# Performance work log

Measured on AMD Instinct MI355X. Metric: run time of the kernel, lower is better.

Reference implementation:

```python
import jax, jax.numpy as jnp
import numpy as np

N_NODES = 100000
N_EDGES = 1200000
N_GRAPHS = 1024
IN_FEATS = 64
HID = 64
BN_EPS = 1e-5


def setup_inputs() -> dict:
    key = jax.random.key(0)
    ks = jax.random.split(key, 20)
    feats = jax.random.normal(ks[0], (N_NODES, IN_FEATS), jnp.float32)
    src = jax.random.randint(ks[1], (N_EDGES,), 0, N_NODES, jnp.int32)
    dst = jax.random.randint(ks[2], (N_EDGES,), 0, N_NODES, jnp.int32)
    graph_ids = jnp.sort(jax.random.randint(ks[3], (N_NODES,), 0, N_GRAPHS, jnp.int32))

    def lin(k, fi, fo):
        s = 1.0 / np.sqrt(fi)
        kw, kb = jax.random.split(k)
        return (jax.random.uniform(kw, (fi, fo), jnp.float32, -s, s),
                jax.random.uniform(kb, (fo,), jnp.float32, -s, s))

    W_self, _ = lin(ks[4], IN_FEATS, HID)
    W_neigh, b_neigh = lin(ks[5], IN_FEATS, HID)
    W1, b1 = lin(ks[6], HID, 128)
    W2, b2 = lin(ks[7], 128, 64)
    W3, b3 = lin(ks[8], 64, 1)

    def bn(k, d):
        k1, k2, k3, k4 = jax.random.split(k, 4)
        return (jax.random.normal(k1, (d,), jnp.float32) * 0.1 + 1.0,
                jax.random.normal(k2, (d,), jnp.float32) * 0.1,
                jax.random.normal(k3, (d,), jnp.float32) * 0.1,
                jax.random.uniform(k4, (d,), jnp.float32, 0.5, 1.5))

    g1, be1, rm1, rv1 = bn(ks[9], 128)
    g2, be2, rm2, rv2 = bn(ks[10], 64)

    return dict(feats=feats, src=src, dst=dst, graph_ids=graph_ids,
                W_self=W_self, W_neigh=W_neigh, b_neigh=b_neigh,
                W1=W1, b1=b1, g1=g1, be1=be1, rm1=rm1, rv1=rv1,
                W2=W2, b2=b2, g2=g2, be2=be2, rm2=rm2, rv2=rv2,
                W3=W3, b3=b3)


def reference(feats, src, dst, graph_ids, W_self, W_neigh, b_neigh,
              W1, b1, g1, be1, rm1, rv1, W2, b2, g2, be2, rm2, rv2, W3, b3):
    # --- SAGEConv (mean aggregator): h = W_self@h_self + W_neigh@mean_neigh + b
    deg = jax.ops.segment_sum(jnp.ones((src.shape[0],), feats.dtype), dst,
                              num_segments=N_NODES)                      # [N]
    agg = jax.ops.segment_sum(feats[src], dst, num_segments=N_NODES)     # [N, F]
    mean_neigh = agg / jnp.maximum(deg, 1.0)[:, None]
    h = feats @ W_self + mean_neigh @ W_neigh + b_neigh
    h = jax.nn.relu(h)                                                   # activation

    # --- per-graph max readout (dgl.max_nodes)
    hg = jax.ops.segment_max(h, graph_ids, num_segments=N_GRAPHS)        # [G, HID]

    # --- MLP head with eval-mode BatchNorm1d
    def bn(x, g, b, rm, rv):
        return (x - rm) * jax.lax.rsqrt(rv + BN_EPS) * g + b

    x = bn(jax.nn.relu(hg @ W1 + b1), g1, be1, rm1, rv1)
    x = bn(jax.nn.relu(x @ W2 + b2), g2, be2, rm2, rv2)
    return x @ W3 + b3                                                   # [G, n_task]
```

## Files before the change

kernel.cpp:

```cpp
#include <hip/hip_runtime.h>
#include <hip/hip_fp16.h>

#define N_NODES  100000
#define N_EDGES  1200000
#define N_GRAPHS 1024
#define F        64
#define BN_EPS   1e-5f
#define NBUCK    ((N_NODES + 255) / 256)
#define NBLK     512
#define CHUNK    ((N_EDGES + NBLK - 1) / NBLK)
#define MT       128

__global__ __launch_bounds__(256) void chist(const int* __restrict__ dst,
                                             int* __restrict__ Ct,
                                             int* __restrict__ hgbits) {
  __shared__ int lh[NBUCK];
  int b = blockIdx.x, t = threadIdx.x;
  int zidx = b * 256 + t;
  if (zidx < N_GRAPHS * F) hgbits[zidx] = 0;
  for (int i = t; i < NBUCK; i += 256) lh[i] = 0;
  __syncthreads();
  int e0 = b * CHUNK, e1 = e0 + CHUNK;
  if (e1 > N_EDGES) e1 = N_EDGES;
  for (int e = e0 + t; e < e1; e += 256) atomicAdd(&lh[dst[e] >> 8], 1);
  __syncthreads();
  for (int i = t; i < NBUCK; i += 256) Ct[(size_t)b * NBUCK + i] = lh[i];
}

__global__ __launch_bounds__(NBLK) void cscan(int* __restrict__ Ct,
                                              int* __restrict__ bcnt) {
  __shared__ int s[NBLK];
  int i = blockIdx.x, t = threadIdx.x;
  int v = Ct[(size_t)t * NBUCK + i];
  s[t] = v;
  __syncthreads();
  for (int off = 1; off < NBLK; off <<= 1) {
    int u = (t >= off) ? s[t - off] : 0;
    __syncthreads();
    s[t] += u;
    __syncthreads();
  }
  Ct[(size_t)t * NBUCK + i] = s[t] - v;
  if (t == NBLK - 1) bcnt[i] = s[NBLK - 1];
}

__global__ __launch_bounds__(512) void bscan(const int* __restrict__ bcnt,
                                             int* __restrict__ bstart) {
  __shared__ int s[512];
  int t = threadIdx.x;
  int v = (t < NBUCK) ? bcnt[t] : 0;
  s[t] = v;
  __syncthreads();
  for (int off = 1; off < 512; off <<= 1) {
    int u = (t >= off) ? s[t - off] : 0;
    __syncthreads();
    s[t] += u;
    __syncthreads();
  }
  if (t < NBUCK) bstart[t] = s[t] - v;
  if (t == 0) bstart[NBUCK] = N_EDGES;
}

__global__ __launch_bounds__(256) void cscat(const int* __restrict__ src,
                                             const int* __restrict__ dst,
                                             const int* __restrict__ Ct,
                                             const int* __restrict__ bstart,
                                             int* __restrict__ pairs) {
  __shared__ int cur[NBUCK];
  int b = blockIdx.x, t = threadIdx.x;
  for (int i = t; i < NBUCK; i += 256)
    cur[i] = bstart[i] + Ct[(size_t)b * NBUCK + i];
  __syncthreads();
  int e0 = b * CHUNK, e1 = e0 + CHUNK;
  if (e1 > N_EDGES) e1 = N_EDGES;
  for (int e = e0 + t; e < e1; e += 256) {
    int d = dst[e];
    int pos = atomicAdd(&cur[d >> 8], 1);
    pairs[pos] = (int)((((unsigned)d & 255u) << 24) | (unsigned)src[e]);
  }
}

__global__ __launch_bounds__(256) void place(const int* __restrict__ pairs,
                                             const int* __restrict__ bstart,
                                             int* __restrict__ rs,
                                             int* __restrict__ eidx) {
  __shared__ int lh[256];
  __shared__ int cur[256];
  int b = blockIdx.x, t = threadIdx.x;
  int nb0 = b << 8;
  int r0 = bstart[b], r1 = bstart[b + 1];

  lh[t] = 0;
  __syncthreads();
  for (int e = r0 + t; e < r1; e += 256)
    atomicAdd(&lh[((unsigned)pairs[e]) >> 24], 1);
  __syncthreads();

  int v = lh[t];
  cur[t] = v;
  __syncthreads();
  for (int off = 1; off < 256; off <<= 1) {
    int u = (t >= off) ? cur[t - off] : 0;
    __syncthreads();
    cur[t] += u;
    __syncthreads();
  }
  int excl = cur[t] - v;
  int node = nb0 + t;
  if (node < N_NODES) rs[node] = r0 + excl;
  if (b == 0 && t == 0) rs[N_NODES] = N_EDGES;
  __syncthreads();
  cur[t] = r0 + excl;
  __syncthreads();

  for (int e = r0 + t; e < r1; e += 256) {
    unsigned p = (unsigned)pairs[e];
    int pos = atomicAdd(&cur[p >> 24], 1);
    eidx[pos] = (int)(p & 0xFFFFFFu);
  }
}

__global__ __launch_bounds__(256) void gemm_uz(
    const float* __restrict__ feats, const float* __restrict__ Wself,
    const float* __restrict__ Wneigh, __half* __restrict__ Uh,
    __half* __restrict__ Zh) {
  __shared__ float As[MT * 65];
  __shared__ float Ws[64 * 128];
  int t = threadIdx.x;
  int mbase = blockIdx.x * MT;

  for (int i = t; i < 64 * 128; i += 256) {
    int k = i >> 7, j = i & 127;
    Ws[i] = (j < 64) ? Wself[k * 64 + j] : Wneigh[k * 64 + (j - 64)];
  }
#pragma unroll
  for (int s = 0; s < 8; s++) {
    int idx = (s * 256 + t) * 4;
    int m = idx >> 6, k = idx & 63;
    int gm = mbase + m;
    float4 v = (gm < N_NODES) ? *(const float4*)(feats + (size_t)gm * F + k)
                              : make_float4(0.f, 0.f, 0.f, 0.f);
    float* d = As + m * 65 + k;
    d[0] = v.x; d[1] = v.y; d[2] = v.z; d[3] = v.w;
  }
  __syncthreads();

  int wave = t >> 6, lane = t & 63;
  int jq = lane & 3, nq = lane >> 2;
  int half = wave & 1;
  int mb = (wave >> 1) * 64 + 4 * nq;
  int joff = half * 64 + jq * 16;

  float acc[4][16];
#pragma unroll
  for (int i = 0; i < 4; i++)
#pragma unroll
    for (int c = 0; c < 16; c++) acc[i][c] = 0.f;

#pragma unroll 4
  for (int k = 0; k < 64; k++) {
    float a0 = As[(mb + 0) * 65 + k];
    float a1 = As[(mb + 1) * 65 + k];
    float a2 = As[(mb + 2) * 65 + k];
    float a3 = As[(mb + 3) * 65 + k];
    const float4* wr = (const float4*)(Ws + k * 128 + joff);
    float4 w4[4];
    w4[0] = wr[0]; w4[1] = wr[1]; w4[2] = wr[2]; w4[3] = wr[3];
    const float* w = (const float*)w4;
#pragma unroll
    for (int c = 0; c < 16; c++) {
      float wv = w[c];
      acc[0][c] += a0 * wv;
      acc[1][c] += a1 * wv;
      acc[2][c] += a2 * wv;
      acc[3][c] += a3 * wv;
    }
  }

  __half* outp = half ? Zh : Uh;
  int jbase = jq * 16;
#pragma unroll
  for (int i = 0; i < 4; i++) {
    int gm = mbase + mb + i;
    if (gm < N_NODES) {
#pragma unroll
      for (int c4 = 0; c4 < 4; c4++) {
        union { __half h[4]; uint2 u; } pk;
        pk.h[0] = __float2half_rn(acc[i][c4 * 4 + 0]);
        pk.h[1] = __float2half_rn(acc[i][c4 * 4 + 1]);
        pk.h[2] = __float2half_rn(acc[i][c4 * 4 + 2]);
        pk.h[3] = __float2half_rn(acc[i][c4 * 4 + 3]);
        *(uint2*)(outp + (size_t)gm * F + jbase + c4 * 4) = pk.u;
      }
    }
  }
}

__global__ __launch_bounds__(256) void gather_h(
    const __half* __restrict__ Uh, const __half* __restrict__ Zh,
    const int* __restrict__ rs, const int* __restrict__ eidx,
    const float* __restrict__ bneigh, const int* __restrict__ gids,
    int* __restrict__ hgbits) {
  int lane = threadIdx.x & 63;
  int wid  = (blockIdx.x * blockDim.x + threadIdx.x) >> 6;
  const int NW = (2048 * 256) >> 6;
  const int per = (N_NODES + NW - 1) / NW;
  int n0 = wid * per;
  int n1 = n0 + per; if (n1 > N_NODES) n1 = N_NODES;
  if (n0 >= n1) return;
  int fl  = lane & 15;
  int sub = lane >> 4;
  float4 b4 = *(const float4*)(bneigh + 4 * fl);

  int curg = gids[n0];
  float4 gmax = {0.f, 0.f, 0.f, 0.f};

  for (int n = n0; n < n1; n++) {
    uint2 ur = *(const uint2*)(Uh + (size_t)n * F + 4 * fl);
    int r0 = rs[n], r1 = rs[n + 1];
    float sx = 0.f, sy = 0.f, sz = 0.f, sw = 0.f;
    for (int base = r0; base < r1; base += 64) {
      int m = r1 - base; if (m > 64) m = 64;
      int myid = (lane < m) ? eidx[base + lane] : 0;
      for (int jj = 0; jj < m; jj += 16) {
        int j0 = jj + sub;
        int s0 = __shfl(myid, j0);
        int s1 = __shfl(myid, j0 + 4);
        int s2 = __shfl(myid, j0 + 8);
        int s3 = __shfl(myid, j0 + 12);
        uint2 z0 = *(const uint2*)(Zh + (size_t)s0 * F + 4 * fl);
        uint2 z1 = *(const uint2*)(Zh + (size_t)s1 * F + 4 * fl);
        uint2 z2 = *(const uint2*)(Zh + (size_t)s2 * F + 4 * fl);
        uint2 z3 = *(const uint2*)(Zh + (size_t)s3 * F + 4 * fl);
        if (j0 < m) {
          float2 f0 = __half22float2(*(__half2*)&z0.x);
          float2 f1 = __half22float2(*(__half2*)&z0.y);
          sx += f0.x; sy += f0.y; sz += f1.x; sw += f1.y;
        }
        if (j0 + 4 < m) {
          float2 f0 = __half22float2(*(__half2*)&z1.x);
          float2 f1 = __half22float2(*(__half2*)&z1.y);
          sx += f0.x; sy += f0.y; sz += f1.x; sw += f1.y;
        }
        if (j0 + 8 < m) {
          float2 f0 = __half22float2(*(__half2*)&z2.x);
          float2 f1 = __half22float2(*(__half2*)&z2.y);
          sx += f0.x; sy += f0.y; sz += f1.x; sw += f1.y;
        }
        if (j0 + 12 < m) {
          float2 f0 = __half22float2(*(__half2*)&z3.x);
          float2 f1 = __half22float2(*(__half2*)&z3.y);
          sx += f0.x; sy += f0.y; sz += f1.x; sw += f1.y;
        }
      }
    }
    sx += __shfl_xor(sx, 16); sy += __shfl_xor(sy, 16);
    sz += __shfl_xor(sz, 16); sw += __shfl_xor(sw, 16);
    sx += __shfl_xor(sx, 32); sy += __shfl_xor(sy, 32);
    sz += __shfl_xor(sz, 32); sw += __shfl_xor(sw, 32);
    float inv = 1.0f / fmaxf((float)(r1 - r0), 1.0f);

    int g = gids[n];
    if (g != curg) {
      if (sub == 0) {
        int* hp = hgbits + (size_t)curg * F + 4 * fl;
        atomicMax(hp + 0, __float_as_int(gmax.x));
        atomicMax(hp + 1, __float_as_int(gmax.y));
        atomicMax(hp + 2, __float_as_int(gmax.z));
        atomicMax(hp + 3, __float_as_int(gmax.w));
      }
      curg = g; gmax = make_float4(0.f, 0.f, 0.f, 0.f);
    }

    float2 uf0 = __half22float2(*(__half2*)&ur.x);
    float2 uf1 = __half22float2(*(__half2*)&ur.y);
    gmax.x = fmaxf(gmax.x, fmaxf(uf0.x + sx * inv + b4.x, 0.f));
    gmax.y = fmaxf(gmax.y, fmaxf(uf0.y + sy * inv + b4.y, 0.f));
    gmax.z = fmaxf(gmax.z, fmaxf(uf1.x + sz * inv + b4.z, 0.f));
    gmax.w = fmaxf(gmax.w, fmaxf(uf1.y + sw * inv + b4.w, 0.f));
  }
  if (sub == 0) {
    int* hp = hgbits + (size_t)curg * F + 4 * fl;
    atomicMax(hp + 0, __float_as_int(gmax.x));
    atomicMax(hp + 1, __float_as_int(gmax.y));
    atomicMax(hp + 2, __float_as_int(gmax.z));
    atomicMax(hp + 3, __float_as_int(gmax.w));
  }
}

#define GPB 8
__global__ __launch_bounds__(128) void mlp(
    const float* __restrict__ hg,
    const float* __restrict__ W1, const float* __restrict__ b1,
    const float* __restrict__ g1, const float* __restrict__ be1,
    const float* __restrict__ rm1, const float* __restrict__ rv1,
    const float* __restrict__ W2, const float* __restrict__ b2,
    const float* __restrict__ g2, const float* __restrict__ be2,
    const float* __restrict__ rm2, const float* __restrict__ rv2,
    const float* __restrict__ W3, const float* __restrict__ b3,
    float* __restrict__ out) {
  __shared__ float W1s[64 * 128];
  __shared__ float W2s[128 * 64];
  __shared__ float W3s[64];
  __shared__ float sc1[128], sh1[128], b1s[128];
  __shared__ float sc2[64],  sh2[64],  b2s[64];
  __shared__ float s0[64], s1[128], s2[64];
  int t = threadIdx.x;

  for (int i = t; i < 64 * 128; i += 128) W1s[i] = W1[i];
  for (int i = t; i < 128 * 64; i += 128) W2s[i] = W2[i];
  if (t < 64) W3s[t] = W3[t];
  {
    float iv = rsqrtf(rv1[t] + BN_EPS);
    float sc = g1[t] * iv;
    sc1[t] = sc; sh1[t] = be1[t] - rm1[t] * sc; b1s[t] = b1[t];
  }
  if (t < 64) {
    float iv = rsqrtf(rv2[t] + BN_EPS);
    float sc = g2[t] * iv;
    sc2[t] = sc; sh2[t] = be2[t] - rm2[t] * sc; b2s[t] = b2[t];
  }
  __syncthreads();

  for (int gg = 0; gg < GPB; gg++) {
    int g = blockIdx.x * GPB + gg;
    if (t < 64) s0[t] = hg[(size_t)g * F + t];
    __syncthreads();
    {
      float acc = b1s[t];
      for (int i = 0; i < 64; i++) acc += s0[i] * W1s[i * 128 + t];
      acc = fmaxf(acc, 0.0f);
      s1[t] = acc * sc1[t] + sh1[t];
    }
    __syncthreads();
    if (t < 64) {
      float acc = b2s[t];
      for (int i = 0; i < 128; i++) acc += s1[i] * W2s[i * 64 + t];
      acc = fmaxf(acc, 0.0f);
      s2[t] = acc * sc2[t] + sh2[t];
    }
    __syncthreads();
    if (t < 64) {
      float p = s2[t] * W3s[t];
      for (int off = 32; off > 0; off >>= 1) p += __shfl_down(p, off);
      if (t == 0) out[g] = p + b3[0];
    }
    __syncthreads();
  }
}

extern "C" void kernel_launch(void* const* d_in, const int* in_sizes, int n_in,
                              void* d_out, int out_size, void* d_ws, size_t ws_size,
                              hipStream_t stream) {
  const float* feats  = (const float*)d_in[0];
  const int*   src    = (const int*)d_in[1];
  const int*   dst    = (const int*)d_in[2];
  const int*   gids   = (const int*)d_in[3];
  const float* Wself  = (const float*)d_in[4];
  const float* Wneigh = (const float*)d_in[5];
  const float* bneigh = (const float*)d_in[6];
  const float* W1  = (const float*)d_in[7];
  const float* b1  = (const float*)d_in[8];
  const float* g1  = (const float*)d_in[9];
  const float* be1 = (const float*)d_in[10];
  const float* rm1 = (const float*)d_in[11];
  const float* rv1 = (const float*)d_in[12];
  const float* W2  = (const float*)d_in[13];
  const float* b2  = (const float*)d_in[14];
  const float* g2  = (const float*)d_in[15];
  const float* be2 = (const float*)d_in[16];
  const float* rm2 = (const float*)d_in[17];
  const float* rv2 = (const float*)d_in[18];
  const float* W3  = (const float*)d_in[19];
  const float* b3  = (const float*)d_in[20];

  __half* Uh   = (__half*)d_ws;
  __half* Zh   = Uh + (size_t)N_NODES * F;
  int* rs      = (int*)(Zh + (size_t)N_NODES * F);
  int* bstart  = rs + (N_NODES + 1);
  int* bcnt    = bstart + (NBUCK + 1);
  int* hgbits  = bcnt + NBUCK;
  int* Ct      = hgbits + (size_t)N_GRAPHS * F;
  int* pairs   = Ct + (size_t)NBLK * NBUCK;
  int* eidx    = pairs + N_EDGES;

  chist<<<NBLK, 256, 0, stream>>>(dst, Ct, hgbits);
  cscan<<<NBUCK, NBLK, 0, stream>>>(Ct, bcnt);
  bscan<<<1, 512, 0, stream>>>(bcnt, bstart);
  cscat<<<NBLK, 256, 0, stream>>>(src, dst, Ct, bstart, pairs);
  gemm_uz<<<(N_NODES + MT - 1) / MT, 256, 0, stream>>>(feats, Wself, Wneigh,
                                                       Uh, Zh);
  place<<<NBUCK, 256, 0, stream>>>(pairs, bstart, rs, eidx);
  gather_h<<<2048, 256, 0, stream>>>(Uh, Zh, rs, eidx, bneigh, gids, hgbits);
  mlp<<<N_GRAPHS / GPB, 128, 0, stream>>>((const float*)hgbits,
                                          W1, b1, g1, be1, rm1, rv1,
                                          W2, b2, g2, be2, rm2, rv2, W3, b3,
                                          (float*)d_out);
}
```

Baseline: 230.1 us.

## Fuse CSR placement into bucket-level gather with shared-memory atomic accumulation

```diff
diff --git a/kernel.cpp b/kernel.cpp
--- a/kernel.cpp
+++ b/kernel.cpp
@@ -10,6 +10,8 @@
 #define NBLK     512
 #define CHUNK    ((N_EDGES + NBLK - 1) / NBLK)
 #define MT       128
+#define GS       32
+#define ASTRIDE  68
 
 __global__ __launch_bounds__(256) void chist(const int* __restrict__ dst,
                                              int* __restrict__ Ct,
@@ -77,46 +79,6 @@
     int d = dst[e];
     int pos = atomicAdd(&cur[d >> 8], 1);
     pairs[pos] = (int)((((unsigned)d & 255u) << 24) | (unsigned)src[e]);
-  }
-}
-
-__global__ __launch_bounds__(256) void place(const int* __restrict__ pairs,
-                                             const int* __restrict__ bstart,
-                                             int* __restrict__ rs,
-                                             int* __restrict__ eidx) {
-  __shared__ int lh[256];
-  __shared__ int cur[256];
-  int b = blockIdx.x, t = threadIdx.x;
-  int nb0 = b << 8;
-  int r0 = bstart[b], r1 = bstart[b + 1];
-
-  lh[t] = 0;
-  __syncthreads();
-  for (int e = r0 + t; e < r1; e += 256)
-    atomicAdd(&lh[((unsigned)pairs[e]) >> 24], 1);
-  __syncthreads();
-
-  int v = lh[t];
-  cur[t] = v;
-  __syncthreads();
-  for (int off = 1; off < 256; off <<= 1) {
-    int u = (t >= off) ? cur[t - off] : 0;
-    __syncthreads();
-    cur[t] += u;
-    __syncthreads();
-  }
-  int excl = cur[t] - v;
-  int node = nb0 + t;
-  if (node < N_NODES) rs[node] = r0 + excl;
-  if (b == 0 && t == 0) rs[N_NODES] = N_EDGES;
-  __syncthreads();
-  cur[t] = r0 + excl;
-  __syncthreads();
-
-  for (int e = r0 + t; e < r1; e += 256) {
-    unsigned p = (unsigned)pairs[e];
-    int pos = atomicAdd(&cur[p >> 24], 1);
-    eidx[pos] = (int)(p & 0xFFFFFFu);
   }
 }
 
@@ -196,95 +158,83 @@
   }
 }
 
-__global__ __launch_bounds__(256) void gather_h(
+__global__ __launch_bounds__(256) void gather_agg(
     const __half* __restrict__ Uh, const __half* __restrict__ Zh,
-    const int* __restrict__ rs, const int* __restrict__ eidx,
+    const int* __restrict__ pairs, const int* __restrict__ bstart,
     const float* __restrict__ bneigh, const int* __restrict__ gids,
     int* __restrict__ hgbits) {
-  int lane = threadIdx.x & 63;
-  int wid  = (blockIdx.x * blockDim.x + threadIdx.x) >> 6;
-  const int NW = (2048 * 256) >> 6;
-  const int per = (N_NODES + NW - 1) / NW;
-  int n0 = wid * per;
-  int n1 = n0 + per; if (n1 > N_NODES) n1 = N_NODES;
-  if (n0 >= n1) return;
-  int fl  = lane & 15;
-  int sub = lane >> 4;
-  float4 b4 = *(const float4*)(bneigh + 4 * fl);
-
-  int curg = gids[n0];
-  float4 gmax = {0.f, 0.f, 0.f, 0.f};
-
-  for (int n = n0; n < n1; n++) {
-    uint2 ur = *(const uint2*)(Uh + (size_t)n * F + 4 * fl);
-    int r0 = rs[n], r1 = rs[n + 1];
-    float sx = 0.f, sy = 0.f, sz = 0.f, sw = 0.f;
-    for (int base = r0; base < r1; base += 64) {
-      int m = r1 - base; if (m > 64) m = 64;
-      int myid = (lane < m) ? eidx[base + lane] : 0;
-      for (int jj = 0; jj < m; jj += 16) {
-        int j0 = jj + sub;
-        int s0 = __shfl(myid, j0);
-        int s1 = __shfl(myid, j0 + 4);
-        int s2 = __shfl(myid, j0 + 8);
-        int s3 = __shfl(myid, j0 + 12);
-        uint2 z0 = *(const uint2*)(Zh + (size_t)s0 * F + 4 * fl);
-        uint2 z1 = *(const uint2*)(Zh + (size_t)s1 * F + 4 * fl);
-        uint2 z2 = *(const uint2*)(Zh + (size_t)s2 * F + 4 * fl);
-        uint2 z3 = *(const uint2*)(Zh + (size_t)s3 * F + 4 * fl);
-        if (j0 < m) {
-          float2 f0 = __half22float2(*(__half2*)&z0.x);
-          float2 f1 = __half22float2(*(__half2*)&z0.y);
-          sx += f0.x; sy += f0.y; sz += f1.x; sw += f1.y;
-        }
-        if (j0 + 4 < m) {
-          float2 f0 = __half22float2(*(__half2*)&z1.x);
-          float2 f1 = __half22float2(*(__half2*)&z1.y);
-          sx += f0.x; sy += f0.y; sz += f1.x; sw += f1.y;
-        }
-        if (j0 + 8 < m) {
-          float2 f0 = __half22float2(*(__half2*)&z2.x);
-          float2 f1 = __half22float2(*(__half2*)&z2.y);
-          sx += f0.x; sy += f0.y; sz += f1.x; sw += f1.y;
-        }
-        if (j0 + 12 < m) {
-          float2 f0 = __half22float2(*(__half2*)&z3.x);
-          float2 f1 = __half22float2(*(__half2*)&z3.y);
-          sx += f0.x; sy += f0.y; sz += f1.x; sw += f1.y;
-        }
+  __shared__ float acc[256 * ASTRIDE];
+  __shared__ int   degh[256];
+  __shared__ int   gmaxl[GS * 64];
+  int b = blockIdx.x, t = threadIdx.x;
+  int nb0 = b << 8;
+  int nbkt = N_NODES - nb0; if (nbkt > 256) nbkt = 256;
+  int r0 = bstart[b], r1 = bstart[b + 1];
+
+  for (int i = t; i < 256 * ASTRIDE; i += 256) acc[i] = 0.f;
+  degh[t] = 0;
+  for (int i = t; i < GS * 64; i += 256) gmaxl[i] = 0;
+  __syncthreads();
+
+  int q  = t & 15;
+  int eg = t >> 4;
+
+  for (int e = r0 + eg; e < r1; e += 16) {
+    unsigned p = (unsigned)pairs[e];
+    int ld  = (int)(p >> 24);
+    int sid = (int)(p & 0xFFFFFFu);
+    uint2 z = *(const uint2*)(Zh + (size_t)sid * F + 4 * q);
+    float2 f0 = __half22float2(*(__half2*)&z.x);
+    float2 f1 = __half22float2(*(__half2*)&z.y);
+    float* a = acc + ld * ASTRIDE + 4 * q;
+    atomicAdd(a + 0, f0.x);
+    atomicAdd(a + 1, f0.y);
+    atomicAdd(a + 2, f1.x);
+    atomicAdd(a + 3, f1.y);
+    if (q == 0) atomicAdd(&degh[ld], 1);
+  }
+  __syncthreads();
+
+  float4 b4 = *(const float4*)(bneigh + 4 * q);
+  int gid0 = gids[nb0];
+#pragma unroll
+  for (int pass = 0; pass < 16; pass++) {
+    int nl = eg + pass * 16;
+    if (nl < nbkt) {
+      int node = nb0 + nl;
+      float inv = 1.0f / fmaxf((float)degh[nl], 1.0f);
+      uint2 u = *(const uint2*)(Uh + (size_t)node * F + 4 * q);
+      float2 u0 = __half22float2(*(__half2*)&u.x);
+      float2 u1 = __half22float2(*(__half2*)&u.y);
+      const float* a = acc + nl * ASTRIDE + 4 * q;
+      float hx = fmaxf(u0.x + a[0] * inv + b4.x, 0.f);
+      float hy = fmaxf(u0.y + a[1] * inv + b4.y, 0.f);
+      float hz = fmaxf(u1.x + a[2] * inv + b4.z, 0.f);
+      float hw = fmaxf(u1.y + a[3] * inv + b4.w, 0.f);
+      int slot = gids[node] - gid0;
+      if (slot < GS) {
+        int* gm = gmaxl + slot * 64 + 4 * q;
+        atomicMax(gm + 0, __float_as_int(hx));
+        atomicMax(gm + 1, __float_as_int(hy));
+        atomicMax(gm + 2, __float_as_int(hz));
+        atomicMax(gm + 3, __float_as_int(hw));
+      } else {
+        int* hp = hgbits + (size_t)gids[node] * F + 4 * q;
+        atomicMax(hp + 0, __float_as_int(hx));
+        atomicMax(hp + 1, __float_as_int(hy));
+        atomicMax(hp + 2, __float_as_int(hz));
+        atomicMax(hp + 3, __float_as_int(hw));
       }
     }
-    sx += __shfl_xor(sx, 16); sy += __shfl_xor(sy, 16);
-    sz += __shfl_xor(sz, 16); sw += __shfl_xor(sw, 16);
-    sx += __shfl_xor(sx, 32); sy += __shfl_xor(sy, 32);
-    sz += __shfl_xor(sz, 32); sw += __shfl_xor(sw, 32);
-    float inv = 1.0f / fmaxf((float)(r1 - r0), 1.0f);
-
-    int g = gids[n];
-    if (g != curg) {
-      if (sub == 0) {
-        int* hp = hgbits + (size_t)curg * F + 4 * fl;
-        atomicMax(hp + 0, __float_as_int(gmax.x));
-        atomicMax(hp + 1, __float_as_int(gmax.y));
-        atomicMax(hp + 2, __float_as_int(gmax.z));
-        atomicMax(hp + 3, __float_as_int(gmax.w));
-      }
-      curg = g; gmax = make_float4(0.f, 0.f, 0.f, 0.f);
-    }
-
-    float2 uf0 = __half22float2(*(__half2*)&ur.x);
-    float2 uf1 = __half22float2(*(__half2*)&ur.y);
-    gmax.x = fmaxf(gmax.x, fmaxf(uf0.x + sx * inv + b4.x, 0.f));
-    gmax.y = fmaxf(gmax.y, fmaxf(uf0.y + sy * inv + b4.y, 0.f));
-    gmax.z = fmaxf(gmax.z, fmaxf(uf1.x + sz * inv + b4.z, 0.f));
-    gmax.w = fmaxf(gmax.w, fmaxf(uf1.y + sw * inv + b4.w, 0.f));
-  }
-  if (sub == 0) {
-    int* hp = hgbits + (size_t)curg * F + 4 * fl;
-    atomicMax(hp + 0, __float_as_int(gmax.x));
-    atomicMax(hp + 1, __float_as_int(gmax.y));
-    atomicMax(hp + 2, __float_as_int(gmax.z));
-    atomicMax(hp + 3, __float_as_int(gmax.w));
+  }
+  __syncthreads();
+
+  for (int i = t; i < GS * 64; i += 256) {
+    int v = gmaxl[i];
+    if (v != 0) {
+      int slot = i >> 6, f = i & 63;
+      atomicMax(&hgbits[(size_t)(gid0 + slot) * F + f], v);
+    }
   }
 }
 
@@ -376,13 +326,11 @@
 
   __half* Uh   = (__half*)d_ws;
   __half* Zh   = Uh + (size_t)N_NODES * F;
-  int* rs      = (int*)(Zh + (size_t)N_NODES * F);
-  int* bstart  = rs + (N_NODES + 1);
+  int* bstart  = (int*)(Zh + (size_t)N_NODES * F);
   int* bcnt    = bstart + (NBUCK + 1);
   int* hgbits  = bcnt + NBUCK;
   int* Ct      = hgbits + (size_t)N_GRAPHS * F;
   int* pairs   = Ct + (size_t)NBLK * NBUCK;
-  int* eidx    = pairs + N_EDGES;
 
   chist<<<NBLK, 256, 0, stream>>>(dst, Ct, hgbits);
   cscan<<<NBUCK, NBLK, 0, stream>>>(Ct, bcnt);
@@ -390,8 +338,8 @@
   cscat<<<NBLK, 256, 0, stream>>>(src, dst, Ct, bstart, pairs);
   gemm_uz<<<(N_NODES + MT - 1) / MT, 256, 0, stream>>>(feats, Wself, Wneigh,
                                                        Uh, Zh);
-  place<<<NBUCK, 256, 0, stream>>>(pairs, bstart, rs, eidx);
-  gather_h<<<2048, 256, 0, stream>>>(Uh, Zh, rs, eidx, bneigh, gids, hgbits);
+  gather_agg<<<NBUCK, 256, 0, stream>>>(Uh, Zh, pairs, bstart, bneigh,
+                                        gids, hgbits);
   mlp<<<N_GRAPHS / GPB, 128, 0, stream>>>((const float*)hgbits,
                                           W1, b1, g1, be1, rm1, rv1,
                                           W2, b2, g2, be2, rm2, rv2, W3, b3,
```

Result: slower. 703.2 us (+205.6%).

## Fuse histogram into GEMM launch and process four nodes per wavefront in gather

Applied to the files above, without the earlier changes.

```diff
diff --git a/kernel.cpp b/kernel.cpp
--- a/kernel.cpp
+++ b/kernel.cpp
@@ -10,123 +10,33 @@
 #define NBLK     512
 #define CHUNK    ((N_EDGES + NBLK - 1) / NBLK)
 #define MT       128
-
-__global__ __launch_bounds__(256) void chist(const int* __restrict__ dst,
-                                             int* __restrict__ Ct,
-                                             int* __restrict__ hgbits) {
-  __shared__ int lh[NBUCK];
-  int b = blockIdx.x, t = threadIdx.x;
-  int zidx = b * 256 + t;
-  if (zidx < N_GRAPHS * F) hgbits[zidx] = 0;
-  for (int i = t; i < NBUCK; i += 256) lh[i] = 0;
-  __syncthreads();
-  int e0 = b * CHUNK, e1 = e0 + CHUNK;
-  if (e1 > N_EDGES) e1 = N_EDGES;
-  for (int e = e0 + t; e < e1; e += 256) atomicAdd(&lh[dst[e] >> 8], 1);
-  __syncthreads();
-  for (int i = t; i < NBUCK; i += 256) Ct[(size_t)b * NBUCK + i] = lh[i];
-}
-
-__global__ __launch_bounds__(NBLK) void cscan(int* __restrict__ Ct,
-                                              int* __restrict__ bcnt) {
-  __shared__ int s[NBLK];
-  int i = blockIdx.x, t = threadIdx.x;
-  int v = Ct[(size_t)t * NBUCK + i];
-  s[t] = v;
-  __syncthreads();
-  for (int off = 1; off < NBLK; off <<= 1) {
-    int u = (t >= off) ? s[t - off] : 0;
-    __syncthreads();
-    s[t] += u;
-    __syncthreads();
-  }
-  Ct[(size_t)t * NBUCK + i] = s[t] - v;
-  if (t == NBLK - 1) bcnt[i] = s[NBLK - 1];
-}
-
-__global__ __launch_bounds__(512) void bscan(const int* __restrict__ bcnt,
-                                             int* __restrict__ bstart) {
-  __shared__ int s[512];
-  int t = threadIdx.x;
-  int v = (t < NBUCK) ? bcnt[t] : 0;
-  s[t] = v;
-  __syncthreads();
-  for (int off = 1; off < 512; off <<= 1) {
-    int u = (t >= off) ? s[t - off] : 0;
-    __syncthreads();
-    s[t] += u;
-    __syncthreads();
-  }
-  if (t < NBUCK) bstart[t] = s[t] - v;
-  if (t == 0) bstart[NBUCK] = N_EDGES;
-}
-
-__global__ __launch_bounds__(256) void cscat(const int* __restrict__ src,
-                                             const int* __restrict__ dst,
-                                             const int* __restrict__ Ct,
-                                             const int* __restrict__ bstart,
-                                             int* __restrict__ pairs) {
-  __shared__ int cur[NBUCK];
-  int b = blockIdx.x, t = threadIdx.x;
-  for (int i = t; i < NBUCK; i += 256)
-    cur[i] = bstart[i] + Ct[(size_t)b * NBUCK + i];
-  __syncthreads();
-  int e0 = b * CHUNK, e1 = e0 + CHUNK;
-  if (e1 > N_EDGES) e1 = N_EDGES;
-  for (int e = e0 + t; e < e1; e += 256) {
-    int d = dst[e];
-    int pos = atomicAdd(&cur[d >> 8], 1);
-    pairs[pos] = (int)((((unsigned)d & 255u) << 24) | (unsigned)src[e]);
-  }
-}
-
-__global__ __launch_bounds__(256) void place(const int* __restrict__ pairs,
-                                             const int* __restrict__ bstart,
-                                             int* __restrict__ rs,
-                                             int* __restrict__ eidx) {
-  __shared__ int lh[256];
-  __shared__ int cur[256];
-  int b = blockIdx.x, t = threadIdx.x;
-  int nb0 = b << 8;
-  int r0 = bstart[b], r1 = bstart[b + 1];
-
-  lh[t] = 0;
-  __syncthreads();
-  for (int e = r0 + t; e < r1; e += 256)
-    atomicAdd(&lh[((unsigned)pairs[e]) >> 24], 1);
-  __syncthreads();
-
-  int v = lh[t];
-  cur[t] = v;
-  __syncthreads();
-  for (int off = 1; off < 256; off <<= 1) {
-    int u = (t >= off) ? cur[t - off] : 0;
-    __syncthreads();
-    cur[t] += u;
-    __syncthreads();
-  }
-  int excl = cur[t] - v;
-  int node = nb0 + t;
-  if (node < N_NODES) rs[node] = r0 + excl;
-  if (b == 0 && t == 0) rs[N_NODES] = N_EDGES;
-  __syncthreads();
-  cur[t] = r0 + excl;
-  __syncthreads();
-
-  for (int e = r0 + t; e < r1; e += 256) {
-    unsigned p = (unsigned)pairs[e];
-    int pos = atomicAdd(&cur[p >> 24], 1);
-    eidx[pos] = (int)(p & 0xFFFFFFu);
-  }
-}
-
-__global__ __launch_bounds__(256) void gemm_uz(
+#define GEMM_BLOCKS ((N_NODES + MT - 1) / MT)
+
+__global__ __launch_bounds__(256) void prep(
     const float* __restrict__ feats, const float* __restrict__ Wself,
     const float* __restrict__ Wneigh, __half* __restrict__ Uh,
-    __half* __restrict__ Zh) {
-  __shared__ float As[MT * 65];
-  __shared__ float Ws[64 * 128];
+    __half* __restrict__ Zh, const int* __restrict__ dst,
+    int* __restrict__ Ct, int* __restrict__ hgbits) {
+  __shared__ __align__(16) char smraw[MT * 65 * 4 + 64 * 128 * 4];
   int t = threadIdx.x;
+
+  if (blockIdx.x >= GEMM_BLOCKS) {
+    int* lh = (int*)smraw;
+    int b = blockIdx.x - GEMM_BLOCKS;
+    int zidx = b * 256 + t;
+    if (zidx < N_GRAPHS * F) hgbits[zidx] = 0;
+    for (int i = t; i < NBUCK; i += 256) lh[i] = 0;
+    __syncthreads();
+    int e0 = b * CHUNK, e1 = e0 + CHUNK;
+    if (e1 > N_EDGES) e1 = N_EDGES;
+    for (int e = e0 + t; e < e1; e += 256) atomicAdd(&lh[dst[e] >> 8], 1);
+    __syncthreads();
+    for (int i = t; i < NBUCK; i += 256) Ct[(size_t)b * NBUCK + i] = lh[i];
+    return;
+  }
+
+  float* As = (float*)smraw;
+  float* Ws = (float*)(smraw + MT * 65 * 4);
   int mbase = blockIdx.x * MT;
 
   for (int i = t; i < 64 * 128; i += 256) {
@@ -193,6 +103,99 @@
         *(uint2*)(outp + (size_t)gm * F + jbase + c4 * 4) = pk.u;
       }
     }
+  }
+}
+
+__global__ __launch_bounds__(NBLK) void cscan(int* __restrict__ Ct,
+                                              int* __restrict__ bcnt) {
+  __shared__ int s[NBLK];
+  int i = blockIdx.x, t = threadIdx.x;
+  int v = Ct[(size_t)t * NBUCK + i];
+  s[t] = v;
+  __syncthreads();
+  for (int off = 1; off < NBLK; off <<= 1) {
+    int u = (t >= off) ? s[t - off] : 0;
+    __syncthreads();
+    s[t] += u;
+    __syncthreads();
+  }
+  Ct[(size_t)t * NBUCK + i] = s[t] - v;
+  if (t == NBLK - 1) bcnt[i] = s[NBLK - 1];
+}
+
+__global__ __launch_bounds__(512) void bscan(const int* __restrict__ bcnt,
+                                             int* __restrict__ bstart) {
+  __shared__ int s[512];
+  int t = threadIdx.x;
+  int v = (t < NBUCK) ? bcnt[t] : 0;
+  s[t] = v;
+  __syncthreads();
+  for (int off = 1; off < 512; off <<= 1) {
+    int u = (t >= off) ? s[t - off] : 0;
+    __syncthreads();
+    s[t] += u;
+    __syncthreads();
+  }
+  if (t < NBUCK) bstart[t] = s[t] - v;
+  if (t == 0) bstart[NBUCK] = N_EDGES;
+}
+
+__global__ __launch_bounds__(256) void cscat(const int* __restrict__ src,
+                                             const int* __restrict__ dst,
+                                             const int* __restrict__ Ct,
+                                             const int* __restrict__ bstart,
+                                             int* __restrict__ pairs) {
+  __shared__ int cur[NBUCK];
+  int b = blockIdx.x, t = threadIdx.x;
+  for (int i = t; i < NBUCK; i += 256)
+    cur[i] = bstart[i] + Ct[(size_t)b * NBUCK + i];
+  __syncthreads();
+  int e0 = b * CHUNK, e1 = e0 + CHUNK;
+  if (e1 > N_EDGES) e1 = N_EDGES;
+  for (int e = e0 + t; e < e1; e += 256) {
+    int d = dst[e];
+    int pos = atomicAdd(&cur[d >> 8], 1);
+    pairs[pos] = (int)((((unsigned)d & 255u) << 24) | (unsigned)src[e]);
+  }
+}
+
+__global__ __launch_bounds__(256) void place(const int* __restrict__ pairs,
+                                             const int* __restrict__ bstart,
+                                             int* __restrict__ rs,
+                                             int* __restrict__ eidx) {
+  __shared__ int lh[256];
+  __shared__ int cur[256];
+  int b = blockIdx.x, t = threadIdx.x;
+  int nb0 = b << 8;
+  int r0 = bstart[b], r1 = bstart[b + 1];
+
+  lh[t] = 0;
+  __syncthreads();
+  for (int e = r0 + t; e < r1; e += 256)
+    atomicAdd(&lh[((unsigned)pairs[e]) >> 24], 1);
+  __syncthreads();
+
+  int v = lh[t];
+  cur[t] = v;
+  __syncthreads();
+  for (int off = 1; off < 256; off <<= 1) {
+    int u = (t >= off) ? cur[t - off] : 0;
+    __syncthreads();
+    cur[t] += u;
+    __syncthreads();
+  }
+  int excl = cur[t] - v;
+  int node = nb0 + t;
+  if (node < N_NODES) rs[node] = r0 + excl;
+  if (b == 0 && t == 0) rs[N_NODES] = N_EDGES;
+  __syncthreads();
+  cur[t] = r0 + excl;
+  __syncthreads();
+
+  for (int e = r0 + t; e < r1; e += 256) {
+    unsigned p = (unsigned)pairs[e];
+    int pos = atomicAdd(&cur[p >> 24], 1);
+    eidx[pos] = (int)(p & 0xFFFFFFu);
   }
 }
 
@@ -207,79 +210,77 @@
   const int per = (N_NODES + NW - 1) / NW;
   int n0 = wid * per;
   int n1 = n0 + per; if (n1 > N_NODES) n1 = N_NODES;
-  if (n0 >= n1) return;
-  int fl  = lane & 15;
-  int sub = lane >> 4;
+  int g  = lane >> 4;
+  int fl = lane & 15;
+  int gl = g << 4;
   float4 b4 = *(const float4*)(bneigh + 4 * fl);
 
-  int curg = gids[n0];
+  int curg = -1;
   float4 gmax = {0.f, 0.f, 0.f, 0.f};
 
-  for (int n = n0; n < n1; n++) {
+  for (int n = n0 + g; n < n1; n += 4) {
     uint2 ur = *(const uint2*)(Uh + (size_t)n * F + 4 * fl);
     int r0 = rs[n], r1 = rs[n + 1];
     float sx = 0.f, sy = 0.f, sz = 0.f, sw = 0.f;
-    for (int base = r0; base < r1; base += 64) {
-      int m = r1 - base; if (m > 64) m = 64;
-      int myid = (lane < m) ? eidx[base + lane] : 0;
-      for (int jj = 0; jj < m; jj += 16) {
-        int j0 = jj + sub;
-        int s0 = __shfl(myid, j0);
-        int s1 = __shfl(myid, j0 + 4);
-        int s2 = __shfl(myid, j0 + 8);
-        int s3 = __shfl(myid, j0 + 12);
+    for (int base = r0; base < r1; base += 16) {
+      int m = r1 - base; if (m > 16) m = 16;
+      int myid = (fl < m) ? eidx[base + fl] : 0;
+      for (int j = 0; j < m; j += 4) {
+        int s0 = __shfl(myid, gl + j + 0);
+        int s1 = __shfl(myid, gl + j + 1);
+        int s2 = __shfl(myid, gl + j + 2);
+        int s3 = __shfl(myid, gl + j + 3);
         uint2 z0 = *(const uint2*)(Zh + (size_t)s0 * F + 4 * fl);
         uint2 z1 = *(const uint2*)(Zh + (size_t)s1 * F + 4 * fl);
         uint2 z2 = *(const uint2*)(Zh + (size_t)s2 * F + 4 * fl);
         uint2 z3 = *(const uint2*)(Zh + (size_t)s3 * F + 4 * fl);
-        if (j0 < m) {
+        {
           float2 f0 = __half22float2(*(__half2*)&z0.x);
           float2 f1 = __half22float2(*(__half2*)&z0.y);
           sx += f0.x; sy += f0.y; sz += f1.x; sw += f1.y;
         }
-        if (j0 + 4 < m) {
+        if (j + 1 < m) {
           float2 f0 = __half22float2(*(__half2*)&z1.x);
           float2 f1 = __half22float2(*(__half2*)&z1.y);
           sx += f0.x; sy += f0.y; sz += f1.x; sw += f1.y;
         }
-        if (j0 + 8 < m) {
+        if (j + 2 < m) {
           float2 f0 = __half22float2(*(__half2*)&z2.x);
           float2 f1 = __half22float2(*(__half2*)&z2.y);
           sx += f0.x; sy += f0.y; sz += f1.x; sw += f1.y;
         }
-        if (j0 + 12 < m) {
+        if (j + 3 < m) {
           float2 f0 = __half22float2(*(__half2*)&z3.x);
           float2 f1 = __half22float2(*(__half2*)&z3.y);
           sx += f0.x; sy += f0.y; sz += f1.x; sw += f1.y;
         }
       }
     }
-    sx += __shfl_xor(sx, 16); sy += __shfl_xor(sy, 16);
-    sz += __shfl_xor(sz, 16); sw += __shfl_xor(sw, 16);
-    sx += __shfl_xor(sx, 32); sy += __shfl_xor(sy, 32);
-    sz += __shfl_xor(sz, 32); sw += __shfl_xor(sw, 32);
     float inv = 1.0f / fmaxf((float)(r1 - r0), 1.0f);
-
-    int g = gids[n];
-    if (g != curg) {
-      if (sub == 0) {
+    float2 u0 = __half22float2(*(__half2*)&ur.x);
+    float2 u1 = __half22float2(*(__half2*)&ur.y);
+    float hx = fmaxf(u0.x + sx * inv + b4.x, 0.f);
+    float hy = fmaxf(u0.y + sy * inv + b4.y, 0.f);
+    float hz = fmaxf(u1.x + sz * inv + b4.z, 0.f);
+    float hw = fmaxf(u1.y + sw * inv + b4.w, 0.f);
+
+    int gg = gids[n];
+    if (gg != curg) {
+      if (curg >= 0) {
         int* hp = hgbits + (size_t)curg * F + 4 * fl;
         atomicMax(hp + 0, __float_as_int(gmax.x));
         atomicMax(hp + 1, __float_as_int(gmax.y));
         atomicMax(hp + 2, __float_as_int(gmax.z));
         atomicMax(hp + 3, __float_as_int(gmax.w));
       }
-      curg = g; gmax = make_float4(0.f, 0.f, 0.f, 0.f);
-    }
-
-    float2 uf0 = __half22float2(*(__half2*)&ur.x);
-    float2 uf1 = __half22float2(*(__half2*)&ur.y);
-    gmax.x = fmaxf(gmax.x, fmaxf(uf0.x + sx * inv + b4.x, 0.f));
-    gmax.y = fmaxf(gmax.y, fmaxf(uf0.y + sy * inv + b4.y, 0.f));
-    gmax.z = fmaxf(gmax.z, fmaxf(uf1.x + sz * inv + b4.z, 0.f));
-    gmax.w = fmaxf(gmax.w, fmaxf(uf1.y + sw * inv + b4.w, 0.f));
-  }
-  if (sub == 0) {
+      curg = gg; gmax = make_float4(0.f, 0.f, 0.f, 0.f);
+    }
+    gmax.x = fmaxf(gmax.x, hx);
+    gmax.y = fmaxf(gmax.y, hy);
+    gmax.z = fmaxf(gmax.z, hz);
+    gmax.w = fmaxf(gmax.w, hw);
+  }
+  if (curg >= 0) {
     int* hp = hgbits + (size_t)curg * F + 4 * fl;
     atomicMax(hp + 0, __float_as_int(gmax.x));
     atomicMax(hp + 1, __float_as_int(gmax.y));
@@ -384,12 +385,11 @@
   int* pairs   = Ct + (size_t)NBLK * NBUCK;
   int* eidx    = pairs + N_EDGES;
 
-  chist<<<NBLK, 256, 0, stream>>>(dst, Ct, hgbits);
+  prep<<<GEMM_BLOCKS + NBLK, 256, 0, stream>>>(feats, Wself, Wneigh, Uh, Zh,
+                                               dst, Ct, hgbits);
   cscan<<<NBUCK, NBLK, 0, stream>>>(Ct, bcnt);
   bscan<<<1, 512, 0, stream>>>(bcnt, bstart);
   cscat<<<NBLK, 256, 0, stream>>>(src, dst, Ct, bstart, pairs);
-  gemm_uz<<<(N_NODES + MT - 1) / MT, 256, 0, stream>>>(feats, Wself, Wneigh,
-                                                       Uh, Zh);
   place<<<NBUCK, 256, 0, stream>>>(pairs, bstart, rs, eidx);
   gather_h<<<2048, 256, 0, stream>>>(Uh, Zh, rs, eidx, bneigh, gids, hgbits);
   mlp<<<N_GRAPHS / GPB, 128, 0, stream>>>((const float*)hgbits,
```

Result: slower. 243.4 us (+5.8%).

## Fuse CSR build stages into one persistent kernel with software grid barriers

Applied to the files above, without the earlier changes.

```diff
diff --git a/kernel.cpp b/kernel.cpp
--- a/kernel.cpp
+++ b/kernel.cpp
@@ -7,128 +7,23 @@
 #define F        64
 #define BN_EPS   1e-5f
 #define NBUCK    ((N_NODES + 255) / 256)
-#define NBLK     512
-#define CHUNK    ((N_EDGES + NBLK - 1) / NBLK)
+#define NCHUNK   NBUCK
+#define CHUNK    ((N_EDGES + NCHUNK - 1) / NCHUNK)
 #define MT       128
-
-__global__ __launch_bounds__(256) void chist(const int* __restrict__ dst,
-                                             int* __restrict__ Ct,
-                                             int* __restrict__ hgbits) {
-  __shared__ int lh[NBUCK];
-  int b = blockIdx.x, t = threadIdx.x;
-  int zidx = b * 256 + t;
-  if (zidx < N_GRAPHS * F) hgbits[zidx] = 0;
-  for (int i = t; i < NBUCK; i += 256) lh[i] = 0;
-  __syncthreads();
-  int e0 = b * CHUNK, e1 = e0 + CHUNK;
-  if (e1 > N_EDGES) e1 = N_EDGES;
-  for (int e = e0 + t; e < e1; e += 256) atomicAdd(&lh[dst[e] >> 8], 1);
-  __syncthreads();
-  for (int i = t; i < NBUCK; i += 256) Ct[(size_t)b * NBUCK + i] = lh[i];
-}
-
-__global__ __launch_bounds__(NBLK) void cscan(int* __restrict__ Ct,
-                                              int* __restrict__ bcnt) {
-  __shared__ int s[NBLK];
-  int i = blockIdx.x, t = threadIdx.x;
-  int v = Ct[(size_t)t * NBUCK + i];
-  s[t] = v;
-  __syncthreads();
-  for (int off = 1; off < NBLK; off <<= 1) {
-    int u = (t >= off) ? s[t - off] : 0;
-    __syncthreads();
-    s[t] += u;
-    __syncthreads();
-  }
-  Ct[(size_t)t * NBUCK + i] = s[t] - v;
-  if (t == NBLK - 1) bcnt[i] = s[NBLK - 1];
-}
-
-__global__ __launch_bounds__(512) void bscan(const int* __restrict__ bcnt,
-                                             int* __restrict__ bstart) {
-  __shared__ int s[512];
-  int t = threadIdx.x;
-  int v = (t < NBUCK) ? bcnt[t] : 0;
-  s[t] = v;
-  __syncthreads();
-  for (int off = 1; off < 512; off <<= 1) {
-    int u = (t >= off) ? s[t - off] : 0;
-    __syncthreads();
-    s[t] += u;
-    __syncthreads();
-  }
-  if (t < NBUCK) bstart[t] = s[t] - v;
-  if (t == 0) bstart[NBUCK] = N_EDGES;
-}
-
-__global__ __launch_bounds__(256) void cscat(const int* __restrict__ src,
-                                             const int* __restrict__ dst,
-                                             const int* __restrict__ Ct,
-                                             const int* __restrict__ bstart,
-                                             int* __restrict__ pairs) {
-  __shared__ int cur[NBUCK];
-  int b = blockIdx.x, t = threadIdx.x;
-  for (int i = t; i < NBUCK; i += 256)
-    cur[i] = bstart[i] + Ct[(size_t)b * NBUCK + i];
-  __syncthreads();
-  int e0 = b * CHUNK, e1 = e0 + CHUNK;
-  if (e1 > N_EDGES) e1 = N_EDGES;
-  for (int e = e0 + t; e < e1; e += 256) {
-    int d = dst[e];
-    int pos = atomicAdd(&cur[d >> 8], 1);
-    pairs[pos] = (int)((((unsigned)d & 255u) << 24) | (unsigned)src[e]);
-  }
-}
-
-__global__ __launch_bounds__(256) void place(const int* __restrict__ pairs,
-                                             const int* __restrict__ bstart,
-                                             int* __restrict__ rs,
-                                             int* __restrict__ eidx) {
-  __shared__ int lh[256];
-  __shared__ int cur[256];
-  int b = blockIdx.x, t = threadIdx.x;
-  int nb0 = b << 8;
-  int r0 = bstart[b], r1 = bstart[b + 1];
-
-  lh[t] = 0;
-  __syncthreads();
-  for (int e = r0 + t; e < r1; e += 256)
-    atomicAdd(&lh[((unsigned)pairs[e]) >> 24], 1);
-  __syncthreads();
-
-  int v = lh[t];
-  cur[t] = v;
-  __syncthreads();
-  for (int off = 1; off < 256; off <<= 1) {
-    int u = (t >= off) ? cur[t - off] : 0;
-    __syncthreads();
-    cur[t] += u;
-    __syncthreads();
-  }
-  int excl = cur[t] - v;
-  int node = nb0 + t;
-  if (node < N_NODES) rs[node] = r0 + excl;
-  if (b == 0 && t == 0) rs[N_NODES] = N_EDGES;
-  __syncthreads();
-  cur[t] = r0 + excl;
-  __syncthreads();
-
-  for (int e = r0 + t; e < r1; e += 256) {
-    unsigned p = (unsigned)pairs[e];
-    int pos = atomicAdd(&cur[p >> 24], 1);
-    eidx[pos] = (int)(p & 0xFFFFFFu);
-  }
-}
-
-__global__ __launch_bounds__(256) void gemm_uz(
+#define GEMM_BLOCKS ((N_NODES + MT - 1) / MT)
+
+__global__ __launch_bounds__(256) void prep(
     const float* __restrict__ feats, const float* __restrict__ Wself,
     const float* __restrict__ Wneigh, __half* __restrict__ Uh,
-    __half* __restrict__ Zh) {
+    __half* __restrict__ Zh, int* __restrict__ hgbits, int* __restrict__ bar) {
   __shared__ float As[MT * 65];
   __shared__ float Ws[64 * 128];
   int t = threadIdx.x;
+  int zidx = blockIdx.x * 256 + t;
+  if (zidx < N_GRAPHS * F) hgbits[zidx] = 0;
+  if (blockIdx.x == 0 && t < 2) bar[t] = 0;
+
   int mbase = blockIdx.x * MT;
-
   for (int i = t; i < 64 * 128; i += 256) {
     int k = i >> 7, j = i & 127;
     Ws[i] = (j < 64) ? Wself[k * 64 + j] : Wneigh[k * 64 + (j - 64)];
@@ -192,6 +87,127 @@
         pk.h[3] = __float2half_rn(acc[i][c4 * 4 + 3]);
         *(uint2*)(outp + (size_t)gm * F + jbase + c4 * 4) = pk.u;
       }
+    }
+  }
+}
+
+__device__ __forceinline__ void gridbar(int* cnt, int* gen, int nblk) {
+  __syncthreads();
+  if (threadIdx.x == 0) {
+    __threadfence();
+    int g = atomicAdd(gen, 0);
+    if (atomicAdd(cnt, 1) == nblk - 1) {
+      atomicExch(cnt, 0);
+      __threadfence();
+      atomicAdd(gen, 1);
+    } else {
+      while (atomicAdd(gen, 0) == g) __builtin_amdgcn_s_sleep(8);
+    }
+    __threadfence();
+  }
+  __syncthreads();
+}
+
+__global__ __launch_bounds__(256) void csr_build(
+    const int* __restrict__ src, const int* __restrict__ dst,
+    int* __restrict__ Ct, int* __restrict__ bcnt, int* __restrict__ bstart,
+    int* __restrict__ pairs, int* __restrict__ rs, int* __restrict__ eidx,
+    int* __restrict__ bar) {
+  __shared__ int sm[512];
+  int b = blockIdx.x, t = threadIdx.x;
+  int e0 = b * CHUNK, e1 = e0 + CHUNK;
+  if (e1 > N_EDGES) e1 = N_EDGES;
+
+  for (int i = t; i < NBUCK; i += 256) sm[i] = 0;
+  __syncthreads();
+  for (int e = e0 + t; e < e1; e += 256) atomicAdd(&sm[dst[e] >> 8], 1);
+  __syncthreads();
+  for (int i = t; i < NBUCK; i += 256) Ct[(size_t)b * NBUCK + i] = sm[i];
+  gridbar(&bar[0], &bar[1], NCHUNK);
+
+  {
+    int c0 = 2 * t, c1 = 2 * t + 1;
+    int x0 = (c0 < NCHUNK) ? Ct[(size_t)c0 * NBUCK + b] : 0;
+    int x1 = (c1 < NCHUNK) ? Ct[(size_t)c1 * NBUCK + b] : 0;
+    int s = x0 + x1;
+    sm[t] = s;
+    __syncthreads();
+    for (int off = 1; off < 256; off <<= 1) {
+      int u = (t >= off) ? sm[t - off] : 0;
+      __syncthreads();
+      sm[t] += u;
+      __syncthreads();
+    }
+    int excl = sm[t] - s;
+    if (c0 < NCHUNK) Ct[(size_t)c0 * NBUCK + b] = excl;
+    if (c1 < NCHUNK) Ct[(size_t)c1 * NBUCK + b] = excl + x0;
+    if (t == 255) bcnt[b] = sm[255];
+  }
+  gridbar(&bar[0], &bar[1], NCHUNK);
+
+  if (b == 0) {
+    int c0 = 2 * t, c1 = 2 * t + 1;
+    int x0 = (c0 < NBUCK) ? atomicAdd(&bcnt[c0], 0) : 0;
+    int x1 = (c1 < NBUCK) ? atomicAdd(&bcnt[c1], 0) : 0;
+    int s = x0 + x1;
+    sm[t] = s;
+    __syncthreads();
+    for (int off = 1; off < 256; off <<= 1) {
+      int u = (t >= off) ? sm[t - off] : 0;
+      __syncthreads();
+      sm[t] += u;
+      __syncthreads();
+    }
+    int excl = sm[t] - s;
+    if (c0 < NBUCK) bstart[c0] = excl;
+    if (c1 < NBUCK) bstart[c1] = excl + x0;
+    if (t == 0) bstart[NBUCK] = N_EDGES;
+  }
+  gridbar(&bar[0], &bar[1], NCHUNK);
+
+  for (int i = t; i < NBUCK; i += 256)
+    sm[i] = bstart[i] + Ct[(size_t)b * NBUCK + i];
+  __syncthreads();
+  for (int e = e0 + t; e < e1; e += 256) {
+    int d = dst[e];
+    int pos = atomicAdd(&sm[d >> 8], 1);
+    pairs[pos] = (int)((((unsigned)d & 255u) << 24) | (unsigned)src[e]);
+  }
+  gridbar(&bar[0], &bar[1], NCHUNK);
+
+  {
+    int* lh  = sm;
+    int* cur = sm + 256;
+    int nb0 = b << 8;
+    int r0 = bstart[b], r1 = bstart[b + 1];
+
+    lh[t] = 0;
+    __syncthreads();
+    for (int e = r0 + t; e < r1; e += 256)
+      atomicAdd(&lh[((unsigned)pairs[e]) >> 24], 1);
+    __syncthreads();
+
+    int v = lh[t];
+    cur[t] = v;
+    __syncthreads();
+    for (int off = 1; off < 256; off <<= 1) {
+      int u = (t >= off) ? cur[t - off] : 0;
+      __syncthreads();
+      cur[t] += u;
+      __syncthreads();
+    }
+    int excl = cur[t] - v;
+    int node = nb0 + t;
+    if (node < N_NODES) rs[node] = r0 + excl;
+    if (b == 0 && t == 0) rs[N_NODES] = N_EDGES;
+    __syncthreads();
+    cur[t] = r0 + excl;
+    __syncthreads();
+
+    for (int e = r0 + t; e < r1; e += 256) {
+      unsigned p = (unsigned)pairs[e];
+      int pos = atomicAdd(&cur[p >> 24], 1);
+      eidx[pos] = (int)(p & 0xFFFFFFu);
     }
   }
 }
@@ -379,18 +395,16 @@
   int* rs      = (int*)(Zh + (size_t)N_NODES * F);
   int* bstart  = rs + (N_NODES + 1);
   int* bcnt    = bstart + (NBUCK + 1);
-  int* hgbits  = bcnt + NBUCK;
+  int* bar     = bcnt + NBUCK;
+  int* hgbits  = bar + 2;
   int* Ct      = hgbits + (size_t)N_GRAPHS * F;
-  int* pairs   = Ct + (size_t)NBLK * NBUCK;
+  int* pairs   = Ct + (size_t)NCHUNK * NBUCK;
   int* eidx    = pairs + N_EDGES;
 
-  chist<<<NBLK, 256, 0, stream>>>(dst, Ct, hgbits);
-  cscan<<<NBUCK, NBLK, 0, stream>>>(Ct, bcnt);
-  bscan<<<1, 512, 0, stream>>>(bcnt, bstart);
-  cscat<<<NBLK, 256, 0, stream>>>(src, dst, Ct, bstart, pairs);
-  gemm_uz<<<(N_NODES + MT - 1) / MT, 256, 0, stream>>>(feats, Wself, Wneigh,
-                                                       Uh, Zh);
-  place<<<NBUCK, 256, 0, stream>>>(pairs, bstart, rs, eidx);
+  prep<<<GEMM_BLOCKS, 256, 0, stream>>>(feats, Wself, Wneigh, Uh, Zh,
+                                        hgbits, bar);
+  csr_build<<<NCHUNK, 256, 0, stream>>>(src, dst, Ct, bcnt, bstart,
+                                        pairs, rs, eidx, bar);
   gather_h<<<2048, 256, 0, stream>>>(Uh, Zh, rs, eidx, bneigh, gids, hgbits);
   mlp<<<N_GRAPHS / GPB, 128, 0, stream>>>((const float*)hgbits,
                                           W1, b1, g1, be1, rm1, rv1,
```

After: 378.7 us. 1.65x slower.
